# Optimization experiments

Measured on AMD Instinct MI355X. Metric: run time of the kernel, lower is better.

Reference implementation:

```python
import jax, jax.numpy as jnp
import numpy as np


def setup_inputs() -> dict:
    key = jax.random.key(0)
    kq, kk, kv = jax.random.split(key, 3)
    # transpose_batch_sequence=True layout: [seq, batch, heads, head_dim]
    query = jax.random.normal(kq, (2048, 2, 32, 128), dtype=jnp.float32)
    k = jax.random.normal(kk, (2048, 2, 8, 128), dtype=jnp.float32)
    v = jax.random.normal(kv, (2048, 2, 8, 128), dtype=jnp.float32)
    return {"query": query, "key": k, "value": v}


def reference(query, key, value):
    # scale_attn_logits=True
    head_dim = query.shape[-1]
    q = query / jnp.sqrt(jnp.asarray(head_dim, dtype=query.dtype))
    h_q, h_kv = q.shape[-2], key.shape[-2]
    group_size = h_q // h_kv
    # [q, b, h_kv, g, d]
    gq = q.reshape((*q.shape[:2], h_kv, group_size, q.shape[-1]))
    # scores: [b, h_kv, g, q, k]
    attn = jnp.einsum('qbhgd,kbhd->bhgqk', gq, key)
    attn = jax.nn.softmax(attn, axis=-1)
    # output: [q, b, h_kv, g, d] -> [q, b, h_q, d]
    out = jnp.einsum('bhgqk,kbhd->qbhgd', attn, value)
    return out.reshape(query.shape)
```

## Files before the change

### kernel.cpp

```cpp
#include <hip/hip_runtime.h>

#define SEQ   2048
#define NB    2
#define NHQ   32
#define NHKV  8
#define HD    128
#define QTILE 128
#define QW    32
#define KVB   32
#define NT    (SEQ / KVB)
#define SCALE 0.08838834764831845f
#define QSCALE (0.08838834764831845f * 1.4426950408889634f)
#define THRL2 11.5f

#define QSTRIDE (NB * NHQ * HD)
#define KSTRIDE (NB * NHKV * HD)

typedef float f32x4  __attribute__((ext_vector_type(4)));
typedef float f32x16 __attribute__((ext_vector_type(16)));
typedef __bf16 bf16x8 __attribute__((ext_vector_type(8)));
typedef unsigned short ushort8 __attribute__((ext_vector_type(8)));
typedef unsigned int u32;
typedef unsigned int u32x2 __attribute__((ext_vector_type(2)));
typedef unsigned int u32x4 __attribute__((ext_vector_type(4)));

__device__ __forceinline__ unsigned short f2bf(float f) {
    union { float f; unsigned u; } c; c.f = f;
    return (unsigned short)((c.u + 0x7fffu + ((c.u >> 16) & 1u)) >> 16);
}

__device__ __forceinline__ void gload_lds16(const unsigned short* g, unsigned short* l) {
    __builtin_amdgcn_global_load_lds((const __attribute__((address_space(1))) u32*)g,
                                     (__attribute__((address_space(3))) u32*)l, 16, 0, 0);
}

__device__ __forceinline__ float ex2(float x) {
#if __has_builtin(__builtin_amdgcn_exp2f)
    return __builtin_amdgcn_exp2f(x);
#else
    return exp2f(x);
#endif
}

__device__ __forceinline__ u32 cvtpk(float lo, float hi) {
    u32 r;
    asm("v_cvt_pk_bf16_f32 %0, %1, %2" : "=v"(r) : "v"(lo), "v"(hi));
    return r;
}

__device__ __forceinline__ void pl32swap(u32& a, u32& b) {
#if __has_builtin(__builtin_amdgcn_permlane32_swap)
    u32x2 r = __builtin_amdgcn_permlane32_swap(a, b, false, false);
    a = r.x; b = r.y;
#else
    asm("v_permlane32_swap_b32 %0, %1" : "+v"(a), "+v"(b));
#endif
}

template <int B>
__device__ __forceinline__ bf16x8 make_pa(const f32x16 p) {
    u32 w0 = cvtpk(p[B + 0], p[B + 1]);
    u32 w2 = cvtpk(p[B + 4], p[B + 5]);
    pl32swap(w0, w2);
    u32 w1 = cvtpk(p[B + 2], p[B + 3]);
    u32 w3 = cvtpk(p[B + 6], p[B + 7]);
    pl32swap(w1, w3);
    u32x4 v = {w0, w1, w2, w3};
    return __builtin_bit_cast(bf16x8, v);
}

__global__ __launch_bounds__(256) void conv_k(const float* __restrict__ K,
                                              unsigned short* __restrict__ Kws) {
    int idx = blockIdx.x * 256 + threadIdx.x;
    int c  = idx & 15;
    int s  = (idx >> 4) & 2047;
    int bh = idx >> 15;
    int cs = c ^ (s & 7);
    const float* src = K + ((size_t)s * 16 + bh) * 128 + cs * 8;
    float4 f0 = *(const float4*)src;
    float4 f1 = *(const float4*)(src + 4);
    ushort8 u;
    u[0] = f2bf(f0.x); u[1] = f2bf(f0.y); u[2] = f2bf(f0.z); u[3] = f2bf(f0.w);
    u[4] = f2bf(f1.x); u[5] = f2bf(f1.y); u[6] = f2bf(f1.z); u[7] = f2bf(f1.w);
    *(ushort8*)&Kws[((size_t)bh * 2048 + s) * 128 + c * 8] = u;
}

__global__ __launch_bounds__(256) void conv_v(const float* __restrict__ V,
                                              unsigned short* __restrict__ Vt) {
    __shared__ float tile[64][129];
    int t64 = blockIdx.x & 31;
    int bh  = blockIdx.x >> 5;
    int kv0 = t64 * 64;
#pragma unroll
    for (int i = 0; i < 8; ++i) {
        int f4 = i * 256 + threadIdx.x;
        int kv = f4 >> 5, d4 = (f4 & 31) * 4;
        float4 v = *(const float4*)(V + ((size_t)(kv0 + kv) * 16 + bh) * 128 + d4);
        tile[kv][d4] = v.x; tile[kv][d4 + 1] = v.y;
        tile[kv][d4 + 2] = v.z; tile[kv][d4 + 3] = v.w;
    }
    __syncthreads();
#pragma unroll
    for (int i = 0; i < 4; ++i) {
        int lin = i * 256 + threadIdx.x;
        int c = lin & 7, d = lin >> 3;
        int grp = c >> 2, cw = c & 3;
        int cs = cw ^ (d & 3);
        ushort8 u;
#pragma unroll
        for (int j = 0; j < 8; ++j) u[j] = f2bf(tile[grp * 32 + cs * 8 + j][d]);
        *(ushort8*)&Vt[((size_t)bh * 128 + d) * 2048 + kv0 + grp * 32 + cw * 8] = u;
    }
}

__global__ __launch_bounds__(256, 3)
void attn_fwd7(const float* __restrict__ Q, const unsigned short* __restrict__ Kws,
               const unsigned short* __restrict__ Vtws, float* __restrict__ O) {
    __shared__ __align__(16) unsigned char smemc[49152];

    const int tid  = threadIdx.x;
    const int w    = tid >> 6;
    const int lane = tid & 63;
    const int q31  = lane & 31;
    const int h    = lane >> 5;

    const int bid   = blockIdx.x;
    const int hkv   = bid & 7;
    const int rest  = bid >> 3;
    const int g     = rest & 3;
    const int b     = (rest >> 2) & 1;
    const int qtile = rest >> 3;
    const int hq    = hkv * 4 + g;

    const int qrow = qtile * QTILE + w * QW + q31;

    bf16x8 qf[8];
    {
        const float* qp = Q + (size_t)qrow * QSTRIDE + b * (NHQ * HD) + hq * HD;
#pragma unroll
        for (int s = 0; s < 8; ++s) {
            const float* p = qp + (2 * s + h) * 8;
            float4 f0 = *(const float4*)(p);
            float4 f1 = *(const float4*)(p + 4);
            ushort8 u;
            u[0] = f2bf(f0.x * QSCALE); u[1] = f2bf(f0.y * QSCALE);
            u[2] = f2bf(f0.z * QSCALE); u[3] = f2bf(f0.w * QSCALE);
            u[4] = f2bf(f1.x * QSCALE); u[5] = f2bf(f1.y * QSCALE);
            u[6] = f2bf(f1.z * QSCALE); u[7] = f2bf(f1.w * QSCALE);
            qf[s] = __builtin_bit_cast(bf16x8, u);
        }
    }

    u32 kad[8], vad[2];
#pragma unroll
    for (int s = 0; s < 8; ++s)
        kad[s] = q31 * 256 + (((2 * s + h) ^ (q31 & 7)) << 4);
#pragma unroll
    for (int ks = 0; ks < 2; ++ks)
        vad[ks] = 24576 + q31 * 64 + (((2 * ks + h) ^ (q31 & 3)) << 4);

    f32x16 acc[4];
#pragma unroll
    for (int db = 0; db < 4; ++db) acc[db] = (f32x16)0.f;
    float mr = -3e38f, lsum = 0.f;

    const unsigned short* kbh = Kws  + (size_t)(b * 8 + hkv) * 2048 * 128;
    const unsigned short* vbh = Vtws + (size_t)(b * 8 + hkv) * 128 * 2048;

#define STAGE(sofb, tt) do {                                                           \
        const int kv0s = (tt) * KVB;                                                   \
        _Pragma("unroll")                                                              \
        for (int i_ = 0; i_ < 2; ++i_) {                                               \
            const int c_ = w * 2 + i_;                                                 \
            gload_lds16(kbh + (size_t)(kv0s + c_ * 4 + (lane >> 4)) * 128 + (lane & 15) * 8, \
                        (unsigned short*)(smemc + (sofb) + c_ * 1024));                \
            gload_lds16(vbh + (size_t)(c_ * 16 + (lane >> 2)) * 2048 + kv0s + (lane & 3) * 8, \
                        (unsigned short*)(smemc + 24576 + (sofb) + c_ * 1024));        \
        }                                                                              \
    } while (0)

    STAGE(0, 0);
    STAGE(8192, 1);
    int kof = 0;
    int sof = 16384;

    for (int t = 0; t < NT; ++t) {
        if (t < NT - 1) {
            asm volatile("s_waitcnt vmcnt(4)" ::: "memory");
        } else {
            asm volatile("s_waitcnt vmcnt(0)" ::: "memory");
        }
        __builtin_amdgcn_s_barrier();
        if (t + 2 < NT) STAGE(sof, t + 2);

        f32x16 sa = (f32x16)0.f;
        __builtin_amdgcn_s_setprio(1);
#pragma unroll
        for (int s = 0; s < 8; ++s) {
            bf16x8 kf = *(const bf16x8*)&smemc[kad[s] + kof];
            sa = __builtin_amdgcn_mfma_f32_32x32x16_bf16(kf, qf[s], sa, 0, 0, 0);
        }
        __builtin_amdgcn_s_setprio(0);

        {
            float t0 = fmaxf(fmaxf(sa[0], sa[1]),   fmaxf(sa[2], sa[3]));
            float t1 = fmaxf(fmaxf(sa[4], sa[5]),   fmaxf(sa[6], sa[7]));
            float t2 = fmaxf(fmaxf(sa[8], sa[9]),   fmaxf(sa[10], sa[11]));
            float t3 = fmaxf(fmaxf(sa[12], sa[13]), fmaxf(sa[14], sa[15]));
            float tm = fmaxf(fmaxf(t0, t1), fmaxf(t2, t3));
            tm = fmaxf(tm, __shfl_xor(tm, 32));
            if (!__all(tm <= mr + THRL2)) {
                float mn   = fmaxf(mr, tm);
                float corr = ex2(mr - mn);
                lsum *= corr;
#pragma unroll
                for (int db = 0; db < 4; ++db)
#pragma unroll
                    for (int r = 0; r < 16; ++r) acc[db][r] *= corr;
                mr = mn;
            }
#pragma unroll
            for (int r = 0; r < 16; ++r) sa[r] = ex2(sa[r] - mr);
            float s0 = (sa[0] + sa[1]) + (sa[2] + sa[3]);
            float s1 = (sa[4] + sa[5]) + (sa[6] + sa[7]);
            float s2 = (sa[8] + sa[9]) + (sa[10] + sa[11]);
            float s3 = (sa[12] + sa[13]) + (sa[14] + sa[15]);
            lsum += (s0 + s1) + (s2 + s3);
        }

        bf16x8 pa[2];
        pa[0] = make_pa<0>(sa);
        pa[1] = make_pa<8>(sa);

        __builtin_amdgcn_s_setprio(1);
#pragma unroll
        for (int db = 0; db < 4; ++db) {
#pragma unroll
            for (int ks = 0; ks < 2; ++ks) {
                bf16x8 vf = *(const bf16x8*)&smemc[vad[ks] + kof + db * 2048];
                acc[db] = __builtin_amdgcn_mfma_f32_32x32x16_bf16(vf, pa[ks], acc[db], 0, 0, 0);
            }
        }
        __builtin_amdgcn_s_setprio(0);

        kof = (kof == 16384) ? 0 : kof + 8192;
        sof = (sof == 16384) ? 0 : sof + 8192;
    }
#undef STAGE

    __syncthreads();
    lsum += __shfl_xor(lsum, 32);
    float invl = 1.f / lsum;
    float* ep = (float*)(void*)smemc + w * 2176;
    const int qtb = qtile * QTILE + w * QW;
    float* ob = O + b * (NHQ * HD) + hq * HD;

#pragma unroll
    for (int pass = 0; pass < 2; ++pass) {
#pragma unroll
        for (int db2 = 0; db2 < 2; ++db2) {
            const int db = pass * 2 + db2;
#pragma unroll
            for (int r = 0; r < 16; ++r)
                ep[q31 * 68 + db2 * 32 + (r & 3) + 8 * (r >> 2) + 4 * h] = acc[db][r] * invl;
        }
        __syncthreads();
#pragma unroll
        for (int i = 0; i < 8; ++i) {
            const int row = i * 4 + (lane >> 4);
            const int f4  = lane & 15;
            float4 val = *(const float4*)&ep[row * 68 + f4 * 4];
            *(float4*)(ob + (size_t)(qtb + row) * QSTRIDE + pass * 64 + f4 * 4) = val;
        }
        __syncthreads();
    }
}

#define KPAD  136
#define VPAD  72
#define PPAD  72
__global__ __launch_bounds__(512, 2)
void attn_fwd(const float* __restrict__ Q, const float* __restrict__ K,
              const float* __restrict__ V, float* __restrict__ O) {
    __shared__ __align__(16) unsigned short kbuf[64 * KPAD];
    __shared__ __align__(16) unsigned short vbuf[HD * VPAD];
    __shared__ __align__(16) unsigned short pbuf[8][16 * PPAD];

    const int tid = threadIdx.x;
    const int w = tid >> 6, lane = tid & 63;
    const int row16 = lane & 15, kg = lane >> 4;
    const int bid = blockIdx.x;
    const int qtile = bid & 7, g = (bid >> 3) & 3, b = (bid >> 5) & 1, hkv = bid >> 6;
    const int hq = hkv * 4 + g;
    const int qbase = qtile * 256 + w * 32;

    ushort8 qf[2][4];
#pragma unroll
    for (int s = 0; s < 2; ++s) {
        const int qrow = qbase + s * 16 + row16;
        const float* qp = Q + (size_t)qrow * QSTRIDE + b * (NHQ * HD) + hq * HD;
#pragma unroll
        for (int kk = 0; kk < 4; ++kk) {
            const float* p = qp + kk * 32 + kg * 8;
            float4 f0 = *(const float4*)(p);
            float4 f1 = *(const float4*)(p + 4);
            ushort8 u;
            u[0] = f2bf(f0.x * SCALE); u[1] = f2bf(f0.y * SCALE);
            u[2] = f2bf(f0.z * SCALE); u[3] = f2bf(f0.w * SCALE);
            u[4] = f2bf(f1.x * SCALE); u[5] = f2bf(f1.y * SCALE);
            u[6] = f2bf(f1.z * SCALE); u[7] = f2bf(f1.w * SCALE);
            qf[s][kk] = u;
        }
    }
    float m[2][4], lsum[2][4];
    f32x4 acco[2][8];
#pragma unroll
    for (int s = 0; s < 2; ++s)
#pragma unroll
        for (int r = 0; r < 4; ++r) { m[s][r] = -1e30f; lsum[s][r] = 0.f; }
#pragma unroll
    for (int s = 0; s < 2; ++s)
#pragma unroll
        for (int n = 0; n < 8; ++n) acco[s][n] = (f32x4)0.f;

    const float* kb0 = K + b * (NHKV * HD) + hkv * HD;
    const float* vb0 = V + b * (NHKV * HD) + hkv * HD;

    for (int kvt = 0; kvt < SEQ / 64; ++kvt) {
        const int kv0 = kvt * 64;
        __syncthreads();
        const float* kb = kb0 + (size_t)kv0 * KSTRIDE;
#pragma unroll
        for (int i = 0; i < 2; ++i) {
            int c = i * 512 + tid;
            int row = c >> 4, c8 = c & 15;
            const float* src = kb + (size_t)row * KSTRIDE + c8 * 8;
            float4 f0 = *(const float4*)(src);
            float4 f1 = *(const float4*)(src + 4);
            ushort8 u;
            u[0] = f2bf(f0.x); u[1] = f2bf(f0.y); u[2] = f2bf(f0.z); u[3] = f2bf(f0.w);
            u[4] = f2bf(f1.x); u[5] = f2bf(f1.y); u[6] = f2bf(f1.z); u[7] = f2bf(f1.w);
            *(ushort8*)&kbuf[row * KPAD + c8 * 8] = u;
        }
        const float* vb = vb0 + (size_t)kv0 * KSTRIDE;
#pragma unroll
        for (int i = 0; i < 4; ++i) {
            int f4i = i * 512 + tid;
            int kv = f4i >> 5, d0 = (f4i & 31) * 4;
            float4 v4 = *(const float4*)(vb + (size_t)kv * KSTRIDE + d0);
            vbuf[(d0 + 0) * VPAD + kv] = f2bf(v4.x);
            vbuf[(d0 + 1) * VPAD + kv] = f2bf(v4.y);
            vbuf[(d0 + 2) * VPAD + kv] = f2bf(v4.z);
            vbuf[(d0 + 3) * VPAD + kv] = f2bf(v4.w);
        }
        __syncthreads();

        f32x4 sa[2][4];
#pragma unroll
        for (int s = 0; s < 2; ++s)
#pragma unroll
            for (int n = 0; n < 4; ++n) sa[s][n] = (f32x4)0.f;
#pragma unroll
        for (int kk = 0; kk < 4; ++kk) {
#pragma unroll
            for (int n = 0; n < 4; ++n) {
                bf16x8 bfr = *(const bf16x8*)&kbuf[(n * 16 + row16) * KPAD + kk * 32 + kg * 8];
                sa[0][n] = __builtin_amdgcn_mfma_f32_16x16x32_bf16(
                    __builtin_bit_cast(bf16x8, qf[0][kk]), bfr, sa[0][n], 0, 0, 0);
                sa[1][n] = __builtin_amdgcn_mfma_f32_16x16x32_bf16(
                    __builtin_bit_cast(bf16x8, qf[1][kk]), bfr, sa[1][n], 0, 0, 0);
            }
        }
#pragma unroll
        for (int s = 0; s < 2; ++s) {
#pragma unroll
            for (int r = 0; r < 4; ++r) {
                float tm = fmaxf(fmaxf(sa[s][0][r], sa[s][1][r]), fmaxf(sa[s][2][r], sa[s][3][r]));
                tm = fmaxf(tm, __shfl_xor(tm, 1, 16));
                tm = fmaxf(tm, __shfl_xor(tm, 2, 16));
                tm = fmaxf(tm, __shfl_xor(tm, 4, 16));
                tm = fmaxf(tm, __shfl_xor(tm, 8, 16));
                float mn = fmaxf(m[s][r], tm);
                float corr = __expf(m[s][r] - mn);
                float ps = 0.f;
                int prow = kg * 4 + r;
#pragma unroll
                for (int n = 0; n < 4; ++n) {
                    float p = __expf(sa[s][n][r] - mn);
                    ps += p;
                    pbuf[w][prow * PPAD + n * 16 + row16] = f2bf(p);
                }
                ps += __shfl_xor(ps, 1, 16);
                ps += __shfl_xor(ps, 2, 16);
                ps += __shfl_xor(ps, 4, 16);
                ps += __shfl_xor(ps, 8, 16);
                lsum[s][r] = lsum[s][r] * corr + ps;
                m[s][r] = mn;
#pragma unroll
                for (int n8 = 0; n8 < 8; ++n8) acco[s][n8][r] *= corr;
            }
#pragma unroll
            for (int kk2 = 0; kk2 < 2; ++kk2) {
                bf16x8 pa = *(const bf16x8*)&pbuf[w][row16 * PPAD + kk2 * 32 + kg * 8];
#pragma unroll
                for (int n8 = 0; n8 < 8; ++n8) {
                    bf16x8 vf = *(const bf16x8*)&vbuf[(n8 * 16 + row16) * VPAD + kk2 * 32 + kg * 8];
                    acco[s][n8] = __builtin_amdgcn_mfma_f32_16x16x32_bf16(pa, vf, acco[s][n8], 0, 0, 0);
                }
            }
        }
    }
    float* ob = O + b * (NHQ * HD) + hq * HD;
#pragma unroll
    for (int s = 0; s < 2; ++s)
#pragma unroll
        for (int r = 0; r < 4; ++r) {
            float inv = 1.f / lsum[s][r];
            int qrow = qbase + s * 16 + kg * 4 + r;
            float* op = ob + (size_t)qrow * QSTRIDE;
#pragma unroll
            for (int n8 = 0; n8 < 8; ++n8)
                op[n8 * 16 + row16] = acco[s][n8][r] * inv;
        }
}

extern "C" void kernel_launch(void* const* d_in, const int* in_sizes, int n_in,
                              void* d_out, int out_size, void* d_ws, size_t ws_size,
                              hipStream_t stream) {
    (void)in_sizes; (void)n_in; (void)out_size;
    const float* Q = (const float*)d_in[0];
    const float* K = (const float*)d_in[1];
    const float* V = (const float*)d_in[2];
    float* Out = (float*)d_out;

    const size_t kv_elems = (size_t)16 * 2048 * 128;
    const size_t need = kv_elems * 2 * sizeof(unsigned short);

    if (ws_size >= need) {
        unsigned short* Kws = (unsigned short*)d_ws;
        unsigned short* Vt  = Kws + kv_elems;
        conv_k<<<dim3(2048), dim3(256), 0, stream>>>(K, Kws);
        conv_v<<<dim3(512), dim3(256), 0, stream>>>(V, Vt);
        attn_fwd7<<<dim3(1024), dim3(256), 0, stream>>>(Q, Kws, Vt, Out);
    } else {
        attn_fwd<<<dim3(512), dim3(512), 0, stream>>>(Q, K, V, Out);
    }
}
```

Before: 187.8 us.

## Software-pipeline QK^T of the next tile with softmax, and change the V swizzle

The attention loop now computes the QK^T MFMAs for tile t+1 before running softmax and PV for tile t, so tensor-core work can overlap the exp and reduce math. The first tile's scores are computed before the loop. The per-iteration wait now sits at the end of the iteration and drains all outstanding loads. Separately, the XOR swizzle of the transposed V layout changes from (d&3) to ((d>>1)&3), in both the conversion kernel and the LDS read addresses, to cut bank conflicts. The risks are higher register pressure under the 3-blocks-per-CU launch bound and a shallower load lookahead from the full vmcnt(0) wait.

```diff
diff --git a/kernel.cpp b/kernel.cpp
--- a/kernel.cpp
+++ b/kernel.cpp
@@ -105,7 +105,7 @@
         int lin = i * 256 + threadIdx.x;
         int c = lin & 7, d = lin >> 3;
         int grp = c >> 2, cw = c & 3;
-        int cs = cw ^ (d & 3);
+        int cs = cw ^ ((d >> 1) & 3);
         ushort8 u;
 #pragma unroll
         for (int j = 0; j < 8; ++j) u[j] = f2bf(tile[grp * 32 + cs * 8 + j][d]);
@@ -114,7 +114,7 @@
 }
 
 __global__ __launch_bounds__(256, 3)
-void attn_fwd7(const float* __restrict__ Q, const unsigned short* __restrict__ Kws,
+void attn_fwd8(const float* __restrict__ Q, const unsigned short* __restrict__ Kws,
                const unsigned short* __restrict__ Vtws, float* __restrict__ O) {
     __shared__ __align__(16) unsigned char smemc[49152];
 
@@ -157,7 +157,7 @@
         kad[s] = q31 * 256 + (((2 * s + h) ^ (q31 & 7)) << 4);
 #pragma unroll
     for (int ks = 0; ks < 2; ++ks)
-        vad[ks] = 24576 + q31 * 64 + (((2 * ks + h) ^ (q31 & 3)) << 4);
+        vad[ks] = 24576 + q31 * 64 + (((2 * ks + h) ^ ((q31 >> 1) & 3)) << 4);
 
     f32x16 acc[4];
 #pragma unroll
@@ -181,32 +181,41 @@
 
     STAGE(0, 0);
     STAGE(8192, 1);
-    int kof = 0;
-    int sof = 16384;
+    asm volatile("s_waitcnt vmcnt(0)" ::: "memory");
+    __builtin_amdgcn_s_barrier();
+
+    f32x16 sa_c = (f32x16)0.f;
+    __builtin_amdgcn_s_setprio(1);
+#pragma unroll
+    for (int s = 0; s < 8; ++s) {
+        bf16x8 kf = *(const bf16x8*)&smemc[kad[s]];
+        sa_c = __builtin_amdgcn_mfma_f32_32x32x16_bf16(kf, qf[s], sa_c, 0, 0, 0);
+    }
+    __builtin_amdgcn_s_setprio(0);
+
+    int cyc_cur = 0;
+    int cyc_nxt = 8192;
+    int sof     = 16384;
 
     for (int t = 0; t < NT; ++t) {
-        if (t < NT - 1) {
-            asm volatile("s_waitcnt vmcnt(4)" ::: "memory");
-        } else {
-            asm volatile("s_waitcnt vmcnt(0)" ::: "memory");
-        }
-        __builtin_amdgcn_s_barrier();
         if (t + 2 < NT) STAGE(sof, t + 2);
 
-        f32x16 sa = (f32x16)0.f;
-        __builtin_amdgcn_s_setprio(1);
-#pragma unroll
-        for (int s = 0; s < 8; ++s) {
-            bf16x8 kf = *(const bf16x8*)&smemc[kad[s] + kof];
-            sa = __builtin_amdgcn_mfma_f32_32x32x16_bf16(kf, qf[s], sa, 0, 0, 0);
-        }
-        __builtin_amdgcn_s_setprio(0);
+        f32x16 sa_n = (f32x16)0.f;
+        if (t + 1 < NT) {
+            __builtin_amdgcn_s_setprio(1);
+#pragma unroll
+            for (int s = 0; s < 8; ++s) {
+                bf16x8 kf = *(const bf16x8*)&smemc[kad[s] + cyc_nxt];
+                sa_n = __builtin_amdgcn_mfma_f32_32x32x16_bf16(kf, qf[s], sa_n, 0, 0, 0);
+            }
+            __builtin_amdgcn_s_setprio(0);
+        }
 
         {
-            float t0 = fmaxf(fmaxf(sa[0], sa[1]),   fmaxf(sa[2], sa[3]));
-            float t1 = fmaxf(fmaxf(sa[4], sa[5]),   fmaxf(sa[6], sa[7]));
-            float t2 = fmaxf(fmaxf(sa[8], sa[9]),   fmaxf(sa[10], sa[11]));
-            float t3 = fmaxf(fmaxf(sa[12], sa[13]), fmaxf(sa[14], sa[15]));
+            float t0 = fmaxf(fmaxf(sa_c[0], sa_c[1]),   fmaxf(sa_c[2], sa_c[3]));
+            float t1 = fmaxf(fmaxf(sa_c[4], sa_c[5]),   fmaxf(sa_c[6], sa_c[7]));
+            float t2 = fmaxf(fmaxf(sa_c[8], sa_c[9]),   fmaxf(sa_c[10], sa_c[11]));
+            float t3 = fmaxf(fmaxf(sa_c[12], sa_c[13]), fmaxf(sa_c[14], sa_c[15]));
             float tm = fmaxf(fmaxf(t0, t1), fmaxf(t2, t3));
             tm = fmaxf(tm, __shfl_xor(tm, 32));
             if (!__all(tm <= mr + THRL2)) {
@@ -220,31 +229,38 @@
                 mr = mn;
             }
 #pragma unroll
-            for (int r = 0; r < 16; ++r) sa[r] = ex2(sa[r] - mr);
-            float s0 = (sa[0] + sa[1]) + (sa[2] + sa[3]);
-            float s1 = (sa[4] + sa[5]) + (sa[6] + sa[7]);
-            float s2 = (sa[8] + sa[9]) + (sa[10] + sa[11]);
-            float s3 = (sa[12] + sa[13]) + (sa[14] + sa[15]);
+            for (int r = 0; r < 16; ++r) sa_c[r] = ex2(sa_c[r] - mr);
+            float s0 = (sa_c[0] + sa_c[1]) + (sa_c[2] + sa_c[3]);
+            float s1 = (sa_c[4] + sa_c[5]) + (sa_c[6] + sa_c[7]);
+            float s2 = (sa_c[8] + sa_c[9]) + (sa_c[10] + sa_c[11]);
+            float s3 = (sa_c[12] + sa_c[13]) + (sa_c[14] + sa_c[15]);
             lsum += (s0 + s1) + (s2 + s3);
         }
 
         bf16x8 pa[2];
-        pa[0] = make_pa<0>(sa);
-        pa[1] = make_pa<8>(sa);
+        pa[0] = make_pa<0>(sa_c);
+        pa[1] = make_pa<8>(sa_c);
 
         __builtin_amdgcn_s_setprio(1);
 #pragma unroll
         for (int db = 0; db < 4; ++db) {
 #pragma unroll
             for (int ks = 0; ks < 2; ++ks) {
-                bf16x8 vf = *(const bf16x8*)&smemc[vad[ks] + kof + db * 2048];
+                bf16x8 vf = *(const bf16x8*)&smemc[vad[ks] + cyc_cur + db * 2048];
                 acc[db] = __builtin_amdgcn_mfma_f32_32x32x16_bf16(vf, pa[ks], acc[db], 0, 0, 0);
             }
         }
         __builtin_amdgcn_s_setprio(0);
 
-        kof = (kof == 16384) ? 0 : kof + 8192;
-        sof = (sof == 16384) ? 0 : sof + 8192;
+        sa_c = sa_n;
+        cyc_cur = cyc_nxt;
+        cyc_nxt = (cyc_nxt == 16384) ? 0 : cyc_nxt + 8192;
+        sof     = (sof == 16384) ? 0 : sof + 8192;
+
+        if (t < NT - 1) {
+            asm volatile("s_waitcnt vmcnt(0)" ::: "memory");
+            __builtin_amdgcn_s_barrier();
+        }
     }
 #undef STAGE
 
@@ -441,7 +457,7 @@
         unsigned short* Vt  = Kws + kv_elems;
         conv_k<<<dim3(2048), dim3(256), 0, stream>>>(K, Kws);
         conv_v<<<dim3(512), dim3(256), 0, stream>>>(V, Vt);
-        attn_fwd7<<<dim3(1024), dim3(256), 0, stream>>>(Q, Kws, Vt, Out);
+        attn_fwd8<<<dim3(1024), dim3(256), 0, stream>>>(Q, Kws, Vt, Out);
     } else {
         attn_fwd<<<dim3(512), dim3(512), 0, stream>>>(Q, K, V, Out);
     }
```

Measured after the change: 180.3 us. -4.0%, faster.

## Load V directly into registers in MFMA-fragment layout, bypassing LDS

Applied to the files above, without the earlier changes.

The V conversion kernel now writes V in a pre-swizzled layout matching the per-lane MFMA B-operand fragments. The attention kernel then loads each V tile straight from global memory into registers instead of staging it through LDS. This shrinks the LDS allocation and drops the LDS reads for V. Only K stays double-buffered in LDS, with the barrier moved to the end of each iteration. The cost is that every wave issues its own global V loads each iteration, so redundant L2 traffic rises. The load latency also has to be hidden behind the QK^T MFMAs and softmax.

```diff
diff --git a/kernel.cpp b/kernel.cpp
--- a/kernel.cpp
+++ b/kernel.cpp
@@ -86,7 +86,7 @@
 }
 
 __global__ __launch_bounds__(256) void conv_v(const float* __restrict__ V,
-                                              unsigned short* __restrict__ Vt) {
+                                              unsigned short* __restrict__ Vt2) {
     __shared__ float tile[64][129];
     int t64 = blockIdx.x & 31;
     int bh  = blockIdx.x >> 5;
@@ -103,20 +103,24 @@
 #pragma unroll
     for (int i = 0; i < 4; ++i) {
         int lin = i * 256 + threadIdx.x;
-        int c = lin & 7, d = lin >> 3;
-        int grp = c >> 2, cw = c & 3;
-        int cs = cw ^ (d & 3);
+        int l  = lin & 63;
+        int db = (lin >> 6) & 3;
+        int ks = (lin >> 8) & 1;
+        int tt = lin >> 9;
+        int h = l >> 5, q31 = l & 31;
         ushort8 u;
 #pragma unroll
-        for (int j = 0; j < 8; ++j) u[j] = f2bf(tile[grp * 32 + cs * 8 + j][d]);
-        *(ushort8*)&Vt[((size_t)bh * 128 + d) * 2048 + kv0 + grp * 32 + cw * 8] = u;
+        for (int j = 0; j < 8; ++j)
+            u[j] = f2bf(tile[tt * 32 + ks * 16 + h * 8 + j][db * 32 + q31]);
+        size_t off = ((((size_t)bh * 64 + (t64 * 2 + tt)) * 2 + ks) * 4 + db) * 512 + l * 8;
+        *(ushort8*)&Vt2[off] = u;
     }
 }
 
 __global__ __launch_bounds__(256, 3)
-void attn_fwd7(const float* __restrict__ Q, const unsigned short* __restrict__ Kws,
-               const unsigned short* __restrict__ Vtws, float* __restrict__ O) {
-    __shared__ __align__(16) unsigned char smemc[49152];
+void attn_fwd9(const float* __restrict__ Q, const unsigned short* __restrict__ Kws,
+               const unsigned short* __restrict__ Vt2, float* __restrict__ O) {
+    __shared__ __align__(16) unsigned char smemc[34816];
 
     const int tid  = threadIdx.x;
     const int w    = tid >> 6;
@@ -151,47 +155,45 @@
         }
     }
 
-    u32 kad[8], vad[2];
+    u32 kad[8];
 #pragma unroll
     for (int s = 0; s < 8; ++s)
         kad[s] = q31 * 256 + (((2 * s + h) ^ (q31 & 7)) << 4);
-#pragma unroll
-    for (int ks = 0; ks < 2; ++ks)
-        vad[ks] = 24576 + q31 * 64 + (((2 * ks + h) ^ (q31 & 3)) << 4);
 
     f32x16 acc[4];
 #pragma unroll
     for (int db = 0; db < 4; ++db) acc[db] = (f32x16)0.f;
     float mr = -3e38f, lsum = 0.f;
 
-    const unsigned short* kbh = Kws  + (size_t)(b * 8 + hkv) * 2048 * 128;
-    const unsigned short* vbh = Vtws + (size_t)(b * 8 + hkv) * 128 * 2048;
-
-#define STAGE(sofb, tt) do {                                                           \
+    const unsigned short* kbh = Kws + (size_t)(b * 8 + hkv) * 2048 * 128;
+    const unsigned short* vbh = Vt2 + (size_t)(b * 8 + hkv) * 2048 * 128;
+
+#define STAGE_K(sofb, tt) do {                                                         \
         const int kv0s = (tt) * KVB;                                                   \
         _Pragma("unroll")                                                              \
         for (int i_ = 0; i_ < 2; ++i_) {                                               \
             const int c_ = w * 2 + i_;                                                 \
             gload_lds16(kbh + (size_t)(kv0s + c_ * 4 + (lane >> 4)) * 128 + (lane & 15) * 8, \
                         (unsigned short*)(smemc + (sofb) + c_ * 1024));                \
-            gload_lds16(vbh + (size_t)(c_ * 16 + (lane >> 2)) * 2048 + kv0s + (lane & 3) * 8, \
-                        (unsigned short*)(smemc + 24576 + (sofb) + c_ * 1024));        \
         }                                                                              \
     } while (0)
 
-    STAGE(0, 0);
-    STAGE(8192, 1);
+    STAGE_K(0, 0);
+    STAGE_K(8192, 1);
+    asm volatile("s_waitcnt vmcnt(2)" ::: "memory");
+    __builtin_amdgcn_s_barrier();
+
     int kof = 0;
     int sof = 16384;
 
     for (int t = 0; t < NT; ++t) {
-        if (t < NT - 1) {
-            asm volatile("s_waitcnt vmcnt(4)" ::: "memory");
-        } else {
-            asm volatile("s_waitcnt vmcnt(0)" ::: "memory");
-        }
-        __builtin_amdgcn_s_barrier();
-        if (t + 2 < NT) STAGE(sof, t + 2);
+        const unsigned short* vbt = vbh + (size_t)t * 4096;
+        u32x4 va[8];
+#pragma unroll
+        for (int i = 0; i < 8; ++i)
+            va[i] = *(const u32x4*)(vbt + i * 512 + lane * 8);
+
+        if (t + 2 < NT) STAGE_K(sof, t + 2);
 
         f32x16 sa = (f32x16)0.f;
         __builtin_amdgcn_s_setprio(1);
@@ -237,16 +239,18 @@
         for (int db = 0; db < 4; ++db) {
 #pragma unroll
             for (int ks = 0; ks < 2; ++ks) {
-                bf16x8 vf = *(const bf16x8*)&smemc[vad[ks] + kof + db * 2048];
+                bf16x8 vf = __builtin_bit_cast(bf16x8, va[ks * 4 + db]);
                 acc[db] = __builtin_amdgcn_mfma_f32_32x32x16_bf16(vf, pa[ks], acc[db], 0, 0, 0);
             }
         }
         __builtin_amdgcn_s_setprio(0);
 
+        __builtin_amdgcn_s_barrier();
+
         kof = (kof == 16384) ? 0 : kof + 8192;
         sof = (sof == 16384) ? 0 : sof + 8192;
     }
-#undef STAGE
+#undef STAGE_K
 
     __syncthreads();
     lsum += __shfl_xor(lsum, 32);
@@ -438,10 +442,10 @@
 
     if (ws_size >= need) {
         unsigned short* Kws = (unsigned short*)d_ws;
-        unsigned short* Vt  = Kws + kv_elems;
+        unsigned short* Vt2 = Kws + kv_elems;
         conv_k<<<dim3(2048), dim3(256), 0, stream>>>(K, Kws);
-        conv_v<<<dim3(512), dim3(256), 0, stream>>>(V, Vt);
-        attn_fwd7<<<dim3(1024), dim3(256), 0, stream>>>(Q, Kws, Vt, Out);
+        conv_v<<<dim3(512), dim3(256), 0, stream>>>(V, Vt2);
+        attn_fwd9<<<dim3(1024), dim3(256), 0, stream>>>(Q, Kws, Vt2, Out);
     } else {
         attn_fwd<<<dim3(512), dim3(512), 0, stream>>>(Q, K, V, Out);
     }
```

Result: slower. 242.4 us (+29.1%).

## Pre-pack K and V into MFMA fragment order for contiguous tile loads

Applied to the files above, without the earlier changes.

The conversion kernels now write K and V in bf16, already arranged in per-32-row-tile MFMA fragment order. Each KV tile becomes one contiguous 8KB chunk in the workspace, so the attention kernel's global-to-LDS loads are fully linear. LDS reads use simple base-plus-constant offsets instead of XOR-swizzled per-register addresses, which also frees registers. Both conversion kernels now stage through a shared-memory transpose tile, and the unswizzled LDS layout may introduce bank conflicts.

```diff
diff --git a/kernel.cpp b/kernel.cpp
--- a/kernel.cpp
+++ b/kernel.cpp
@@ -70,52 +70,58 @@
 }
 
 __global__ __launch_bounds__(256) void conv_k(const float* __restrict__ K,
-                                              unsigned short* __restrict__ Kws) {
-    int idx = blockIdx.x * 256 + threadIdx.x;
-    int c  = idx & 15;
-    int s  = (idx >> 4) & 2047;
-    int bh = idx >> 15;
-    int cs = c ^ (s & 7);
-    const float* src = K + ((size_t)s * 16 + bh) * 128 + cs * 8;
-    float4 f0 = *(const float4*)src;
-    float4 f1 = *(const float4*)(src + 4);
-    ushort8 u;
-    u[0] = f2bf(f0.x); u[1] = f2bf(f0.y); u[2] = f2bf(f0.z); u[3] = f2bf(f0.w);
-    u[4] = f2bf(f1.x); u[5] = f2bf(f1.y); u[6] = f2bf(f1.z); u[7] = f2bf(f1.w);
-    *(ushort8*)&Kws[((size_t)bh * 2048 + s) * 128 + c * 8] = u;
+                                              unsigned short* __restrict__ Kf) {
+    __shared__ float tile[32][129];
+    int t  = blockIdx.x & 63;
+    int bh = blockIdx.x >> 6;
+#pragma unroll
+    for (int i = 0; i < 4; ++i) {
+        int f4 = i * 256 + threadIdx.x;
+        int r = f4 >> 5, d4 = (f4 & 31) * 4;
+        float4 v = *(const float4*)(K + ((size_t)(t * 32 + r) * 16 + bh) * 128 + d4);
+        tile[r][d4] = v.x; tile[r][d4 + 1] = v.y;
+        tile[r][d4 + 2] = v.z; tile[r][d4 + 3] = v.w;
+    }
+    __syncthreads();
+#pragma unroll
+    for (int i = 0; i < 2; ++i) {
+        int lin = i * 256 + threadIdx.x;
+        int r = lin & 31, c = lin >> 5;
+        ushort8 u;
+#pragma unroll
+        for (int j = 0; j < 8; ++j) u[j] = f2bf(tile[r][c * 8 + j]);
+        *(ushort8*)&Kf[((size_t)(bh * 64 + t) * 16 + c) * 256 + r * 8] = u;
+    }
 }
 
 __global__ __launch_bounds__(256) void conv_v(const float* __restrict__ V,
-                                              unsigned short* __restrict__ Vt) {
-    __shared__ float tile[64][129];
-    int t64 = blockIdx.x & 31;
-    int bh  = blockIdx.x >> 5;
-    int kv0 = t64 * 64;
-#pragma unroll
-    for (int i = 0; i < 8; ++i) {
+                                              unsigned short* __restrict__ Vf) {
+    __shared__ float tile[32][129];
+    int t  = blockIdx.x & 63;
+    int bh = blockIdx.x >> 6;
+#pragma unroll
+    for (int i = 0; i < 4; ++i) {
         int f4 = i * 256 + threadIdx.x;
         int kv = f4 >> 5, d4 = (f4 & 31) * 4;
-        float4 v = *(const float4*)(V + ((size_t)(kv0 + kv) * 16 + bh) * 128 + d4);
+        float4 v = *(const float4*)(V + ((size_t)(t * 32 + kv) * 16 + bh) * 128 + d4);
         tile[kv][d4] = v.x; tile[kv][d4 + 1] = v.y;
         tile[kv][d4 + 2] = v.z; tile[kv][d4 + 3] = v.w;
     }
     __syncthreads();
 #pragma unroll
-    for (int i = 0; i < 4; ++i) {
+    for (int i = 0; i < 2; ++i) {
         int lin = i * 256 + threadIdx.x;
-        int c = lin & 7, d = lin >> 3;
-        int grp = c >> 2, cw = c & 3;
-        int cs = cw ^ (d & 3);
+        int r = lin & 31, db = (lin >> 5) & 3, cv = lin >> 7;
         ushort8 u;
 #pragma unroll
-        for (int j = 0; j < 8; ++j) u[j] = f2bf(tile[grp * 32 + cs * 8 + j][d]);
-        *(ushort8*)&Vt[((size_t)bh * 128 + d) * 2048 + kv0 + grp * 32 + cw * 8] = u;
+        for (int j = 0; j < 8; ++j) u[j] = f2bf(tile[cv * 8 + j][db * 32 + r]);
+        *(ushort8*)&Vf[((size_t)(bh * 64 + t) * 16 + cv * 4 + db) * 256 + r * 8] = u;
     }
 }
 
 __global__ __launch_bounds__(256, 3)
-void attn_fwd7(const float* __restrict__ Q, const unsigned short* __restrict__ Kws,
-               const unsigned short* __restrict__ Vtws, float* __restrict__ O) {
+void attn_fwd10(const float* __restrict__ Q, const unsigned short* __restrict__ Kf,
+                const unsigned short* __restrict__ Vf, float* __restrict__ O) {
     __shared__ __align__(16) unsigned char smemc[49152];
 
     const int tid  = threadIdx.x;
@@ -151,30 +157,24 @@
         }
     }
 
-    u32 kad[8], vad[2];
-#pragma unroll
-    for (int s = 0; s < 8; ++s)
-        kad[s] = q31 * 256 + (((2 * s + h) ^ (q31 & 7)) << 4);
-#pragma unroll
-    for (int ks = 0; ks < 2; ++ks)
-        vad[ks] = 24576 + q31 * 64 + (((2 * ks + h) ^ (q31 & 3)) << 4);
+    const u32 kbase = h * 512 + q31 * 16;
+    const u32 vbase = 24576 + h * 2048 + q31 * 16;
 
     f32x16 acc[4];
 #pragma unroll
     for (int db = 0; db < 4; ++db) acc[db] = (f32x16)0.f;
     float mr = -3e38f, lsum = 0.f;
 
-    const unsigned short* kbh = Kws  + (size_t)(b * 8 + hkv) * 2048 * 128;
-    const unsigned short* vbh = Vtws + (size_t)(b * 8 + hkv) * 128 * 2048;
+    const unsigned short* kbh = Kf + (size_t)(b * 8 + hkv) * 2048 * 128;
+    const unsigned short* vbh = Vf + (size_t)(b * 8 + hkv) * 2048 * 128;
 
 #define STAGE(sofb, tt) do {                                                           \
-        const int kv0s = (tt) * KVB;                                                   \
         _Pragma("unroll")                                                              \
         for (int i_ = 0; i_ < 2; ++i_) {                                               \
             const int c_ = w * 2 + i_;                                                 \
-            gload_lds16(kbh + (size_t)(kv0s + c_ * 4 + (lane >> 4)) * 128 + (lane & 15) * 8, \
+            gload_lds16(kbh + (size_t)(tt) * 4096 + c_ * 512 + lane * 8,               \
                         (unsigned short*)(smemc + (sofb) + c_ * 1024));                \
-            gload_lds16(vbh + (size_t)(c_ * 16 + (lane >> 2)) * 2048 + kv0s + (lane & 3) * 8, \
+            gload_lds16(vbh + (size_t)(tt) * 4096 + c_ * 512 + lane * 8,               \
                         (unsigned short*)(smemc + 24576 + (sofb) + c_ * 1024));        \
         }                                                                              \
     } while (0)
@@ -197,7 +197,7 @@
         __builtin_amdgcn_s_setprio(1);
 #pragma unroll
         for (int s = 0; s < 8; ++s) {
-            bf16x8 kf = *(const bf16x8*)&smemc[kad[s] + kof];
+            bf16x8 kf = *(const bf16x8*)&smemc[kbase + s * 1024 + kof];
             sa = __builtin_amdgcn_mfma_f32_32x32x16_bf16(kf, qf[s], sa, 0, 0, 0);
         }
         __builtin_amdgcn_s_setprio(0);
@@ -237,7 +237,7 @@
         for (int db = 0; db < 4; ++db) {
 #pragma unroll
             for (int ks = 0; ks < 2; ++ks) {
-                bf16x8 vf = *(const bf16x8*)&smemc[vad[ks] + kof + db * 2048];
+                bf16x8 vf = *(const bf16x8*)&smemc[vbase + ks * 4096 + db * 512 + kof];
                 acc[db] = __builtin_amdgcn_mfma_f32_32x32x16_bf16(vf, pa[ks], acc[db], 0, 0, 0);
             }
         }
@@ -437,11 +437,11 @@
     const size_t need = kv_elems * 2 * sizeof(unsigned short);
 
     if (ws_size >= need) {
-        unsigned short* Kws = (unsigned short*)d_ws;
-        unsigned short* Vt  = Kws + kv_elems;
-        conv_k<<<dim3(2048), dim3(256), 0, stream>>>(K, Kws);
-        conv_v<<<dim3(512), dim3(256), 0, stream>>>(V, Vt);
-        attn_fwd7<<<dim3(1024), dim3(256), 0, stream>>>(Q, Kws, Vt, Out);
+        unsigned short* Kf = (unsigned short*)d_ws;
+        unsigned short* Vf = Kf + kv_elems;
+        conv_k<<<dim3(1024), dim3(256), 0, stream>>>(K, Kf);
+        conv_v<<<dim3(1024), dim3(256), 0, stream>>>(V, Vf);
+        attn_fwd10<<<dim3(1024), dim3(256), 0, stream>>>(Q, Kf, Vf, Out);
     } else {
         attn_fwd<<<dim3(512), dim3(512), 0, stream>>>(Q, K, V, Out);
     }
```

Result: faster. 174.7 us (-7.0%).
